# Kernel optimization log

Measured on AMD Instinct MI355X. Metric: run time of the kernel, lower is better.

## Reference

```python
import jax, jax.numpy as jnp
import numpy as np

N = 100000   # rows of edge_attr == number of graph nodes == number of edges (E == N required by index_add_)
B = 64       # number of graphs
IN_CH, HID, OUT_CH, FC_HID = 128, 128, 128, 256


def setup_inputs() -> dict:
    key = jax.random.key(0)
    ks = jax.random.split(key, 20)
    s = 0.05
    inp = {
        "edge_attr": jax.random.normal(ks[0], (N, 6, 120), dtype=jnp.float32),
        "edge_index": jax.random.randint(ks[1], (2, N), 0, N),
        "batch": jnp.sort(jax.random.randint(ks[2], (N,), 0, B)),
        "num_graphs": B,
        # Conv1d: in=6 -> 16 -> 32, k=5, pad=2
        "conv1_w": jax.random.normal(ks[3], (16, 6, 5), dtype=jnp.float32) * s,
        "conv1_b": jnp.zeros((16,), jnp.float32),
        "conv2_w": jax.random.normal(ks[4], (32, 16, 5), dtype=jnp.float32) * s,
        "conv2_b": jnp.zeros((32,), jnp.float32),
        # fc: 32*120 -> in_channels
        "fc_w": jax.random.normal(ks[5], (IN_CH, 32 * 120), dtype=jnp.float32) * s,
        "fc_b": jnp.zeros((IN_CH,), jnp.float32),
        # GCNConv layers (weight as [out, in], like torch Linear)
        "gcn1_w": jax.random.normal(ks[6], (HID, IN_CH), dtype=jnp.float32) * s,
        "gcn1_b": jnp.zeros((HID,), jnp.float32),
        "gcn2_w": jax.random.normal(ks[7], (OUT_CH, HID), dtype=jnp.float32) * s,
        "gcn2_b": jnp.zeros((OUT_CH,), jnp.float32),
        # MLP head
        "fc1_w": jax.random.normal(ks[8], (FC_HID, OUT_CH), dtype=jnp.float32) * s,
        "fc1_b": jnp.zeros((FC_HID,), jnp.float32),
        "fc2_w": jax.random.normal(ks[9], (OUT_CH, FC_HID), dtype=jnp.float32) * s,
        "fc2_b": jnp.zeros((OUT_CH,), jnp.float32),
    }
    return inp


def conv1d(x, w, b):
    # x: [N, C_in, L], w: [C_out, C_in, K], padding=2 (same)
    y = jax.lax.conv_general_dilated(
        x, w, window_strides=(1,), padding=[(2, 2)],
        dimension_numbers=("NCH", "OIH", "NCH"))
    return y + b[None, :, None]


def gcn_conv(x, edge_index, w, b, n_nodes):
    # PyG GCNConv: add self-loops, symmetric normalization deg^-1/2 A_hat deg^-1/2
    src, dst = edge_index[0], edge_index[1]
    loop = jnp.arange(n_nodes)
    src_f = jnp.concatenate([src, loop])
    dst_f = jnp.concatenate([dst, loop])
    deg = jax.ops.segment_sum(jnp.ones_like(src_f, dtype=x.dtype), dst_f,
                              num_segments=n_nodes)
    dinv = jnp.where(deg > 0, jax.lax.rsqrt(deg), 0.0)
    norm = dinv[src_f] * dinv[dst_f]                      # [E+N]
    h = x @ w.T                                           # [N, out]
    msg = h[src_f] * norm[:, None]                        # gather + scale
    return jax.ops.segment_sum(msg, dst_f, num_segments=n_nodes) + b


def reference(edge_attr, edge_index, batch, num_graphs,
              conv1_w, conv1_b, conv2_w, conv2_b, fc_w, fc_b,
              gcn1_w, gcn1_b, gcn2_w, gcn2_b,
              fc1_w, fc1_b, fc2_w, fc2_b):
    n = edge_attr.shape[0]
    x = jax.nn.relu(conv1d(edge_attr, conv1_w, conv1_b))   # [N,16,120]
    x = jax.nn.relu(conv1d(x, conv2_w, conv2_b))           # [N,32,120]
    x = x.reshape(n, -1)                                   # [N,3840]
    x = x @ fc_w.T + fc_b                                  # [N,in_channels]
    x = jax.nn.relu(gcn_conv(x, edge_index, gcn1_w, gcn1_b, n))
    x = gcn_conv(x, edge_index, gcn2_w, gcn2_b, n)         # [N,out_channels]
    # edge-to-batch scatter-add pooling: out[batch[row][e]] += x[e]
    row = edge_index[0]
    out = jax.ops.segment_sum(x, batch[row], num_segments=num_graphs)  # [B,out]
    x = jax.nn.relu(out @ fc1_w.T + fc1_b)
    x = x @ fc2_w.T + fc2_b
    return x
```

## Files before the change

kernel.cpp:

```cpp
#include <hip/hip_runtime.h>

typedef unsigned int u32;
typedef unsigned short u16;
typedef short short8 __attribute__((ext_vector_type(8)));
typedef float floatx4 __attribute__((ext_vector_type(4)));

static __device__ __forceinline__ u32 f2bf(float f) {
  u32 u = __float_as_uint(f);
  return (u + 0x7fffu + ((u >> 16) & 1u)) >> 16;
}


#define X0_ROWS 136
#define X1W_ROWS 66
#define X1W_LDA 24

__global__ __launch_bounds__(256, 2) void k_convfc(
    const float* __restrict__ ea,
    const u32* __restrict__ w1sw, const float* __restrict__ b1,
    const u32* __restrict__ w2sw, const float* __restrict__ b2,
    const u32* __restrict__ fcwsw, const float* __restrict__ fcb,
    float* __restrict__ xfc, int n, int ntiles)
{
  __shared__ __align__(16) u16 sX0[16][X0_ROWS * 8];
  __shared__ __align__(16) u16 sX1[4][X1W_ROWS * X1W_LDA];
  __shared__ __align__(16) u16 sF[32 * 64 * 8];

  const int t = threadIdx.x, lane = t & 63, wv = t >> 6;
  const int quad = lane >> 4, lr = lane & 15;

  for (int i = t; i < 16 * X0_ROWS * 4; i += 256) ((u32*)sX0)[i] = 0;

  short8 w1f[2], w2f[2][3];
#pragma unroll
  for (int kb = 0; kb < 2; ++kb) w1f[kb] = ((const short8*)w1sw)[kb * 64 + lane];
#pragma unroll
  for (int ot = 0; ot < 2; ++ot)
#pragma unroll
    for (int kb = 0; kb < 3; ++kb)
      w2f[ot][kb] = ((const short8*)w2sw)[(ot * 3 + kb) * 64 + lane];

  float b1r[4];
#pragma unroll
  for (int r = 0; r < 4; ++r) b1r[r] = b1[quad * 4 + r];
  const float bv20 = b2[lr], bv21 = b2[16 + lr];

  const int c0 = wv * 16 + lr, c1 = (wv + 4) * 16 + lr;
  const float bv0 = fcb[c0], bv1 = fcb[c1];
  const short8* bw = (const short8*)fcwsw;
  const short8* b0p = bw + ((size_t)wv * 128) * 64 + lane;
  const short8* b1p = bw + ((size_t)(wv + 4) * 128) * 64 + lane;
  const int j2base = wv * 4;
  const float4* eav = (const float4*)ea;

  __syncthreads();

  for (int tile = blockIdx.x; tile < ntiles; tile += gridDim.x) {
    const long node0 = (long)tile * 16;

#pragma unroll
    for (int it = 0; it < 12; ++it) {
      int idx = t + it * 256;
      if (idx < 2880) {
        int nd = idx / 180;
        int rem = idx - nd * 180;
        int c = rem / 30;
        int pq = rem - c * 30;
        long gn = node0 + nd;
        float4 v = make_float4(0.f, 0.f, 0.f, 0.f);
        if (gn < n) v = eav[gn * 180 + rem];
        u16* xp = &sX0[nd][(pq * 4 + 2) * 8 + c];
        xp[0]  = (u16)f2bf(v.x);
        xp[8]  = (u16)f2bf(v.y);
        xp[16] = (u16)f2bf(v.z);
        xp[24] = (u16)f2bf(v.w);
      }
    }
    __syncthreads();

    floatx4 acc0 = {bv0, bv0, bv0, bv0};
    floatx4 acc1 = {bv1, bv1, bv1, bv1};

    for (int r = 0; r < 4; ++r) {
      u16* x1 = sX1[wv];
#pragma unroll 1
      for (int jj = 0; jj < 4; ++jj) {
        const int j2 = j2base + jj;
        const u16* x0n = sX0[j2];
        {
          u32* z = (u32*)(x1 + 16 * X1W_LDA);
#pragma unroll
          for (int i2 = 0; i2 < 7; ++i2) {
            int i = lane + i2 * 64;
            if (i < 444) z[i] = 0;
          }
        }
#pragma unroll
        for (int q4 = 0; q4 < 4; ++q4) {
          const int ptp = 2 * r - 1 + q4;
          if (ptp >= 0 && ptp <= 7) {
            const int row0 = ptp * 16 + lr;
            short8 bx0 = *(const short8*)&x0n[(row0 + quad) * 8];
            short8 bx1 = *(const short8*)&x0n[(row0 + 4 + quad) * 8];
            floatx4 a1 = {b1r[0], b1r[1], b1r[2], b1r[3]};
            a1 = __builtin_amdgcn_mfma_f32_16x16x32_bf16(w1f[0], bx0, a1, 0, 0, 0);
            a1 = __builtin_amdgcn_mfma_f32_16x16x32_bf16(w1f[1], bx1, a1, 0, 0, 0);
            if (ptp < 7 || lr < 8) {
              const int lrow = row0 + 18 - 32 * r;
              u32 lo = f2bf(fmaxf(a1[0], 0.0f)) | (f2bf(fmaxf(a1[1], 0.0f)) << 16);
              u32 hi = f2bf(fmaxf(a1[2], 0.0f)) | (f2bf(fmaxf(a1[3], 0.0f)) << 16);
              *(uint2*)&x1[lrow * X1W_LDA + quad * 4] = make_uint2(lo, hi);
            }
          }
        }
        const int tq = quad >> 1, cq = (quad & 1) * 8;
#pragma unroll
        for (int ptl = 0; ptl < 2; ++ptl) {
          const int lrow0 = ptl * 16 + lr + 16;
          short8 ax0 = *(const short8*)&x1[(lrow0 + tq) * X1W_LDA + cq];
          short8 ax1 = *(const short8*)&x1[(lrow0 + 2 + tq) * X1W_LDA + cq];
          short8 ax2 = *(const short8*)&x1[(lrow0 + 4 + tq) * X1W_LDA + cq];
#pragma unroll
          for (int ot = 0; ot < 2; ++ot) {
            const float bb = ot ? bv21 : bv20;
            floatx4 a2 = {bb, bb, bb, bb};
            a2 = __builtin_amdgcn_mfma_f32_16x16x32_bf16(ax0, w2f[ot][0], a2, 0, 0, 0);
            a2 = __builtin_amdgcn_mfma_f32_16x16x32_bf16(ax1, w2f[ot][1], a2, 0, 0, 0);
            a2 = __builtin_amdgcn_mfma_f32_16x16x32_bf16(ax2, w2f[ot][2], a2, 0, 0, 0);
            u32 lo = f2bf(fmaxf(a2[0], 0.0f)) | (f2bf(fmaxf(a2[1], 0.0f)) << 16);
            u32 hi = f2bf(fmaxf(a2[2], 0.0f)) | (f2bf(fmaxf(a2[3], 0.0f)) << 16);
            const int o = ot * 16 + lr;
            const int s = (ptl * 2 + tq) * 16 + j2;
            const int G = o * 64 + (s ^ (o & 7));
            *(uint2*)&sF[G * 8 + (quad & 1) * 4] = make_uint2(lo, hi);
          }
        }
      }
      __syncthreads();

#pragma unroll 8
      for (int o = 0; o < 32; ++o) {
        short8 a = *(const short8*)&sF[(o * 64 + (lane ^ (o & 7))) * 8];
        const int ks = o * 4 + r;
        short8 bb0 = b0p[(size_t)ks * 64];
        short8 bb1 = b1p[(size_t)ks * 64];
        acc0 = __builtin_amdgcn_mfma_f32_16x16x32_bf16(a, bb0, acc0, 0, 0, 0);
        acc1 = __builtin_amdgcn_mfma_f32_16x16x32_bf16(a, bb1, acc1, 0, 0, 0);
      }
      __syncthreads();
    }

#pragma unroll
    for (int rr = 0; rr < 4; ++rr) {
      long node = node0 + quad * 4 + rr;
      if (node < n) {
        xfc[node * 128 + c0] = acc0[rr];
        xfc[node * 128 + c1] = acc1[rr];
      }
    }
  }
}

__global__ void k_prep(const float* __restrict__ fcw, const float* __restrict__ g1w,
                       const float* __restrict__ g2w, const float* __restrict__ w1,
                       const float* __restrict__ w2,
                       uint4* __restrict__ fcwsw, uint4* __restrict__ g1wsw,
                       uint4* __restrict__ g2wsw, uint4* __restrict__ w1sw,
                       uint4* __restrict__ w2sw,
                       float* __restrict__ dinv, float* __restrict__ pooled, int n)
{
  int gid = blockIdx.x * 256 + threadIdx.x;
  if (gid < 65536) {
    int e = gid, lane = e & 63, t2 = e >> 6, ks = t2 & 127, nt = t2 >> 7;
    int col = nt * 16 + (lane & 15);
    int k0 = ks * 32 + ((lane >> 4) & 3) * 8;
    u32 pk[4];
#pragma unroll
    for (int h = 0; h < 4; ++h) {
      u32 v01[2];
#pragma unroll
      for (int g = 0; g < 2; ++g) {
        int k = k0 + h * 2 + g;
        int o = k >> 7, p = k & 127;
        float v = (p < 120) ? fcw[(size_t)col * 3840 + o * 120 + p] : 0.0f;
        v01[g] = f2bf(v);
      }
      pk[h] = v01[0] | (v01[1] << 16);
    }
    fcwsw[e] = make_uint4(pk[0], pk[1], pk[2], pk[3]);
    return;
  }
  gid -= 65536;
  if (gid < 4096) {
    const float* gw = (gid < 2048) ? g1w : g2w;
    uint4* out = (gid < 2048) ? g1wsw : g2wsw;
    int e = gid & 2047, lane = e & 63;
    int col = (e >> 8) * 16 + (lane & 15);
    int k0 = ((e >> 6) & 3) * 32 + ((lane >> 4) & 3) * 8;
    u32 pk[4];
#pragma unroll
    for (int h = 0; h < 4; ++h)
      pk[h] = f2bf(gw[(size_t)col * 128 + k0 + h * 2]) |
              (f2bf(gw[(size_t)col * 128 + k0 + h * 2 + 1]) << 16);
    out[e] = make_uint4(pk[0], pk[1], pk[2], pk[3]);
    return;
  }
  gid -= 4096;
  if (gid < 128) {
    int e = gid, lane = e & 63, kb = e >> 6, cout = lane & 15;
    int k0 = kb * 32 + ((lane >> 4) & 3) * 8;
    u32 pk[4];
#pragma unroll
    for (int h = 0; h < 4; ++h) {
      u32 v01[2];
#pragma unroll
      for (int g = 0; g < 2; ++g) {
        int k = k0 + h * 2 + g, tap = k >> 3, cin = k & 7;
        float v = (tap < 5 && cin < 6) ? w1[cout * 30 + cin * 5 + tap] : 0.0f;
        v01[g] = f2bf(v);
      }
      pk[h] = v01[0] | (v01[1] << 16);
    }
    w1sw[e] = make_uint4(pk[0], pk[1], pk[2], pk[3]);
    return;
  }
  gid -= 128;
  if (gid < 384) {
    int e = gid, lane = e & 63, t2 = e >> 6;
    int kb = t2 % 3, ot = t2 / 3;
    int o = ot * 16 + (lane & 15);
    int k0 = kb * 32 + ((lane >> 4) & 3) * 8;
    u32 pk[4];
#pragma unroll
    for (int h = 0; h < 4; ++h) {
      u32 v01[2];
#pragma unroll
      for (int g = 0; g < 2; ++g) {
        int k = k0 + h * 2 + g, tap = k >> 4, c = k & 15;
        float v = (tap < 5) ? w2[o * 80 + c * 5 + tap] : 0.0f;
        v01[g] = f2bf(v);
      }
      pk[h] = v01[0] | (v01[1] << 16);
    }
    w2sw[e] = make_uint4(pk[0], pk[1], pk[2], pk[3]);
    return;
  }
  gid -= 384;
  if (gid < n) { dinv[gid] = 1.0f; return; }
  gid -= n;
  if (gid < 8192) pooled[gid] = 0.0f;
}

__global__ __launch_bounds__(256) void k_gcn_gemm(
    const float* __restrict__ X, const u32* __restrict__ wsw,
    const float* __restrict__ bias, const float* __restrict__ dinv,
    float* __restrict__ H, float* __restrict__ Out, int n, int relu)
{
  __shared__ __align__(16) u16 sA[16 * 136];
  __shared__ float sDi[16];
  const int t = threadIdx.x;
  const long node0 = (long)blockIdx.x * 16;
  {
    int nd = t >> 4, k0 = (t & 15) * 8;
    long node = node0 + nd;
    float v[8];
    if (node < n) {
      float4 f0 = *(const float4*)&X[node * 128 + k0];
      float4 f1 = *(const float4*)&X[node * 128 + k0 + 4];
      v[0]=f0.x; v[1]=f0.y; v[2]=f0.z; v[3]=f0.w; v[4]=f1.x; v[5]=f1.y; v[6]=f1.z; v[7]=f1.w;
      if (relu) {
#pragma unroll
        for (int i = 0; i < 8; ++i) v[i] = fmaxf(v[i], 0.0f);
      }
    } else {
#pragma unroll
      for (int i = 0; i < 8; ++i) v[i] = 0.0f;
    }
    u32 pk[4];
#pragma unroll
    for (int h = 0; h < 4; ++h) pk[h] = f2bf(v[2*h]) | (f2bf(v[2*h+1]) << 16);
    *(uint4*)&sA[nd * 136 + k0] = make_uint4(pk[0], pk[1], pk[2], pk[3]);
    if (t < 16) sDi[t] = (node0 + t < n) ? dinv[node0 + t] : 0.0f;
  }
  __syncthreads();
  const int lane = t & 63, wv = t >> 6, quad = lane >> 4, lr = lane & 15;
  short8 af[4];
#pragma unroll
  for (int kb = 0; kb < 4; ++kb)
    af[kb] = *(const short8*)&sA[lr * 136 + kb * 32 + quad * 8];
#pragma unroll
  for (int h = 0; h < 2; ++h) {
    const int nt = wv + h * 4;
    const short8* bp = ((const short8*)wsw) + (nt * 4) * 64 + lane;
    floatx4 acc = {0.0f, 0.0f, 0.0f, 0.0f};
#pragma unroll
    for (int kb = 0; kb < 4; ++kb)
      acc = __builtin_amdgcn_mfma_f32_16x16x32_bf16(af[kb], bp[kb * 64], acc, 0, 0, 0);
    const int col = nt * 16 + lr;
    const float bcol = bias[col];
#pragma unroll
    for (int r = 0; r < 4; ++r) {
      long node = node0 + quad * 4 + r;
      if (node < n) {
        float hv = acc[r];
        float di = sDi[quad * 4 + r];
        H[node * 128 + col] = hv;
        Out[node * 128 + col] = bcol + di * di * hv;
      }
    }
  }
}

__global__ void k_scatter(const float* __restrict__ Hs, float* __restrict__ Out,
                          const int* __restrict__ src, const int* __restrict__ dst,
                          const float* __restrict__ dinv, int n)
{
  const int gid = blockIdx.x * blockDim.x + threadIdx.x;
  const int e = gid >> 6;
  const int lane = gid & 63;
  if (e >= n) return;
  const int s = src[e], d = dst[e];
  const float nrm = dinv[s] * dinv[d];
  const float2 v = *(const float2*)(Hs + (size_t)s * 128 + lane * 2);
  float* o = Out + (size_t)d * 128 + lane * 2;
  unsafeAtomicAdd(o, v.x * nrm);
  unsafeAtomicAdd(o + 1, v.y * nrm);
}

__global__ void k_deg(float* dinv, const int* __restrict__ dst, int n) {
  int i = blockIdx.x * 256 + threadIdx.x; if (i < n) unsafeAtomicAdd(&dinv[dst[i]], 1.0f);
}
__global__ void k_rsqrt(float* p, int n) {
  int i = blockIdx.x * 256 + threadIdx.x; if (i < n) p[i] = rsqrtf(p[i]);
}

__global__ __launch_bounds__(256) void k_pool(const float* __restrict__ X,
    const int* __restrict__ src, const int* __restrict__ batch,
    float* __restrict__ pooled, int n)
{
  __shared__ float sAcc[64 * 128];
  for (int i = threadIdx.x; i < 8192; i += 256) sAcc[i] = 0.0f;
  __syncthreads();
  const int c = threadIdx.x & 127, half = threadIdx.x >> 7;
  for (int e = blockIdx.x * 2 + half; e < n; e += gridDim.x * 2) {
    int g = batch[src[e]];
    atomicAdd(&sAcc[g * 128 + c], X[(size_t)e * 128 + c]);
  }
  __syncthreads();
  for (int i = threadIdx.x; i < 8192; i += 256) unsafeAtomicAdd(&pooled[i], sAcc[i]);
}

__global__ __launch_bounds__(256) void k_mlp(const float* __restrict__ pooled,
    const float* __restrict__ f1w, const float* __restrict__ f1b,
    const float* __restrict__ f2w, const float* __restrict__ f2b,
    float* __restrict__ out)
{
  const int g = blockIdx.x, t = threadIdx.x;
  __shared__ float sP[128];
  __shared__ float sY[256];
  if (t < 128) sP[t] = pooled[g * 128 + t];
  __syncthreads();
  {
    const float* w = f1w + (size_t)t * 128;
    float a = f1b[t];
    for (int k = 0; k < 128; k += 4) {
      float4 w4 = *(const float4*)(w + k);
      a = fmaf(w4.x, sP[k], fmaf(w4.y, sP[k+1], fmaf(w4.z, sP[k+2], fmaf(w4.w, sP[k+3], a))));
    }
    sY[t] = fmaxf(a, 0.0f);
  }
  __syncthreads();
  if (t < 128) {
    const float* w = f2w + (size_t)t * 256;
    float a = f2b[t];
    for (int k = 0; k < 256; k += 4) {
      float4 w4 = *(const float4*)(w + k);
      a = fmaf(w4.x, sY[k], fmaf(w4.y, sY[k+1], fmaf(w4.z, sY[k+2], fmaf(w4.w, sY[k+3], a))));
    }
    out[g * 128 + t] = a;
  }
}

extern "C" void kernel_launch(void* const* d_in, const int* in_sizes, int n_in,
                              void* d_out, int out_size, void* d_ws, size_t ws_size,
                              hipStream_t stream) {
  const float* ea  = (const float*)d_in[0];
  const int* eidx  = (const int*)d_in[1];
  const int* batch = (const int*)d_in[2];
  const float* w1  = (const float*)d_in[4];
  const float* b1  = (const float*)d_in[5];
  const float* w2  = (const float*)d_in[6];
  const float* b2  = (const float*)d_in[7];
  const float* fcw = (const float*)d_in[8];
  const float* fcb = (const float*)d_in[9];
  const float* g1w = (const float*)d_in[10];
  const float* g1b = (const float*)d_in[11];
  const float* g2w = (const float*)d_in[12];
  const float* g2b = (const float*)d_in[13];
  const float* f1w = (const float*)d_in[14];
  const float* f1b = (const float*)d_in[15];
  const float* f2w = (const float*)d_in[16];
  const float* f2b = (const float*)d_in[17];

  const int n = in_sizes[0] / 720;
  const int* src = eidx;
  const int* dst = eidx + n;

  float* A      = (float*)d_ws;
  float* B      = A + (size_t)n * 128;
  float* C      = B + (size_t)n * 128;
  float* dinv   = C + (size_t)n * 128;
  float* pooled = dinv + n;
  u32*   fcwsw  = (u32*)(pooled + 64 * 128);
  u32*   g1wsw  = fcwsw + 65536 * 4;
  u32*   g2wsw  = g1wsw + 2048 * 4;
  u32*   w1sw   = g2wsw + 2048 * 4;
  u32*   w2sw   = w1sw + 128 * 4;

  const int nb_n = (n + 255) / 256;
  const int ntiles = (n + 15) / 16;
  const int prep_total = 65536 + 2048 + 2048 + 128 + 384 + n + 8192;
  k_prep<<<(prep_total + 255) / 256, 256, 0, stream>>>(
      fcw, g1w, g2w, w1, w2, (uint4*)fcwsw, (uint4*)g1wsw, (uint4*)g2wsw,
      (uint4*)w1sw, (uint4*)w2sw, dinv, pooled, n);
  k_deg<<<nb_n, 256, 0, stream>>>(dinv, dst, n);
  k_rsqrt<<<nb_n, 256, 0, stream>>>(dinv, n);

  k_convfc<<<512, 256, 0, stream>>>(ea, w1sw, b1, w2sw, b2, fcwsw, fcb, A, n, ntiles);

  k_gcn_gemm<<<(n + 15) / 16, 256, 0, stream>>>(A, g1wsw, g1b, dinv, B, C, n, 0);
  k_scatter<<<((size_t)n * 64 + 255) / 256, 256, 0, stream>>>(B, C, src, dst, dinv, n);

  k_gcn_gemm<<<(n + 15) / 16, 256, 0, stream>>>(C, g2wsw, g2b, dinv, A, B, n, 1);
  k_scatter<<<((size_t)n * 64 + 255) / 256, 256, 0, stream>>>(A, B, src, dst, dinv, n);

  k_pool<<<256, 256, 0, stream>>>(B, src, batch, pooled, n);
  k_mlp<<<64, 256, 0, stream>>>(pooled, f1w, f1b, f2w, f2b, (float*)d_out);
}
```

Measured before the change: 1.125 ms.

## Use hardware bf16 pack, restructure input staging, and zero only needed padding rows

Replaces the software round-to-nearest bf16 conversion with the v_cvt_pk_bf16_f32 instruction throughout. The edge_attr load becomes a per-position gather of the six channels, written as one 16-byte LDS store per row instead of four scattered 2-byte stores, at the cost of scalar strided global loads instead of float4 loads. The per-iteration zeroing of the conv1 scratch buffer is replaced by zeroing only the boundary rows at r==0 and r==3, and the r loop is fully unrolled. This relies on the remaining rows always being overwritten by the conv1 stage.

```diff
diff --git a/kernel.cpp b/kernel.cpp
--- a/kernel.cpp
+++ b/kernel.cpp
@@ -8,6 +8,11 @@
 static __device__ __forceinline__ u32 f2bf(float f) {
   u32 u = __float_as_uint(f);
   return (u + 0x7fffu + ((u >> 16) & 1u)) >> 16;
+}
+static __device__ __forceinline__ u32 cvtpk(float lo, float hi) {
+  u32 r;
+  asm("v_cvt_pk_bf16_f32 %0, %1, %2" : "=v"(r) : "v"(lo), "v"(hi));
+  return r;
 }
 
 
@@ -51,7 +56,6 @@
   const short8* b0p = bw + ((size_t)wv * 128) * 64 + lane;
   const short8* b1p = bw + ((size_t)(wv + 4) * 128) * 64 + lane;
   const int j2base = wv * 4;
-  const float4* eav = (const float4*)ea;
 
   __syncthreads();
 
@@ -59,21 +63,19 @@
     const long node0 = (long)tile * 16;
 
 #pragma unroll
-    for (int it = 0; it < 12; ++it) {
+    for (int it = 0; it < 8; ++it) {
       int idx = t + it * 256;
-      if (idx < 2880) {
-        int nd = idx / 180;
-        int rem = idx - nd * 180;
-        int c = rem / 30;
-        int pq = rem - c * 30;
+      int nd = idx >> 7, p = idx & 127;
+      if (p < 120) {
         long gn = node0 + nd;
-        float4 v = make_float4(0.f, 0.f, 0.f, 0.f);
-        if (gn < n) v = eav[gn * 180 + rem];
-        u16* xp = &sX0[nd][(pq * 4 + 2) * 8 + c];
-        xp[0]  = (u16)f2bf(v.x);
-        xp[8]  = (u16)f2bf(v.y);
-        xp[16] = (u16)f2bf(v.z);
-        xp[24] = (u16)f2bf(v.w);
+        float v0 = 0.f, v1 = 0.f, v2 = 0.f, v3 = 0.f, v4 = 0.f, v5 = 0.f;
+        if (gn < n) {
+          const float* base = ea + (size_t)gn * 720 + p;
+          v0 = base[0];   v1 = base[120]; v2 = base[240];
+          v3 = base[360]; v4 = base[480]; v5 = base[600];
+        }
+        u32 w0 = cvtpk(v0, v1), w1 = cvtpk(v2, v3), w2 = cvtpk(v4, v5);
+        *(uint4*)&sX0[nd][(p + 2) * 8] = make_uint4(w0, w1, w2, 0u);
       }
     }
     __syncthreads();
@@ -81,20 +83,23 @@
     floatx4 acc0 = {bv0, bv0, bv0, bv0};
     floatx4 acc1 = {bv1, bv1, bv1, bv1};
 
+#pragma unroll
     for (int r = 0; r < 4; ++r) {
       u16* x1 = sX1[wv];
+      if (r == 0) {
+        if (lane < 24) ((u32*)(x1 + 16 * X1W_LDA))[lane] = 0;
+      } else if (r == 3) {
+        u32* z = (u32*)(x1 + 42 * X1W_LDA);
+#pragma unroll
+        for (int i2 = 0; i2 < 3; ++i2) {
+          int i = lane + i2 * 64;
+          if (i < 132) z[i] = 0;
+        }
+      }
 #pragma unroll 1
       for (int jj = 0; jj < 4; ++jj) {
         const int j2 = j2base + jj;
         const u16* x0n = sX0[j2];
-        {
-          u32* z = (u32*)(x1 + 16 * X1W_LDA);
-#pragma unroll
-          for (int i2 = 0; i2 < 7; ++i2) {
-            int i = lane + i2 * 64;
-            if (i < 444) z[i] = 0;
-          }
-        }
 #pragma unroll
         for (int q4 = 0; q4 < 4; ++q4) {
           const int ptp = 2 * r - 1 + q4;
@@ -107,8 +112,8 @@
             a1 = __builtin_amdgcn_mfma_f32_16x16x32_bf16(w1f[1], bx1, a1, 0, 0, 0);
             if (ptp < 7 || lr < 8) {
               const int lrow = row0 + 18 - 32 * r;
-              u32 lo = f2bf(fmaxf(a1[0], 0.0f)) | (f2bf(fmaxf(a1[1], 0.0f)) << 16);
-              u32 hi = f2bf(fmaxf(a1[2], 0.0f)) | (f2bf(fmaxf(a1[3], 0.0f)) << 16);
+              u32 lo = cvtpk(fmaxf(a1[0], 0.0f), fmaxf(a1[1], 0.0f));
+              u32 hi = cvtpk(fmaxf(a1[2], 0.0f), fmaxf(a1[3], 0.0f));
               *(uint2*)&x1[lrow * X1W_LDA + quad * 4] = make_uint2(lo, hi);
             }
           }
@@ -127,8 +132,8 @@
             a2 = __builtin_amdgcn_mfma_f32_16x16x32_bf16(ax0, w2f[ot][0], a2, 0, 0, 0);
             a2 = __builtin_amdgcn_mfma_f32_16x16x32_bf16(ax1, w2f[ot][1], a2, 0, 0, 0);
             a2 = __builtin_amdgcn_mfma_f32_16x16x32_bf16(ax2, w2f[ot][2], a2, 0, 0, 0);
-            u32 lo = f2bf(fmaxf(a2[0], 0.0f)) | (f2bf(fmaxf(a2[1], 0.0f)) << 16);
-            u32 hi = f2bf(fmaxf(a2[2], 0.0f)) | (f2bf(fmaxf(a2[3], 0.0f)) << 16);
+            u32 lo = cvtpk(fmaxf(a2[0], 0.0f), fmaxf(a2[1], 0.0f));
+            u32 hi = cvtpk(fmaxf(a2[2], 0.0f), fmaxf(a2[3], 0.0f));
             const int o = ot * 16 + lr;
             const int s = (ptl * 2 + tq) * 16 + j2;
             const int G = o * 64 + (s ^ (o & 7));
@@ -278,7 +283,7 @@
     }
     u32 pk[4];
 #pragma unroll
-    for (int h = 0; h < 4; ++h) pk[h] = f2bf(v[2*h]) | (f2bf(v[2*h+1]) << 16);
+    for (int h = 0; h < 4; ++h) pk[h] = cvtpk(v[2*h], v[2*h+1]);
     *(uint4*)&sA[nd * 136 + k0] = make_uint4(pk[0], pk[1], pk[2], pk[3]);
     if (t < 16) sDi[t] = (node0 + t < n) ? dinv[node0 + t] : 0.0f;
   }
```

Measured after the change: 1.144 ms. No clear change (+1.7%).
